# Optimization experiments

Measured on AMD Instinct MI355X. Metric: run time of the kernel, lower is better.

## Reference

```python
import jax, jax.numpy as jnp
import numpy as np

C_S, C_Z, H, P_QK, P_V, L = 384, 128, 12, 4, 8, 768
D = C_S // H
OUT_DIM = C_S + H * P_V * 3 + H * C_Z


def setup_inputs() -> dict:
    key = jax.random.key(0)
    ks = jax.random.split(key, 16)
    sc = lambda fan_in: 1.0 / np.sqrt(fan_in)
    inp = {
        'single': jax.random.normal(ks[0], (L, C_S), jnp.float32),
        'pair': jax.random.normal(ks[1], (L, L, C_Z), jnp.float32),
        'rots': jax.random.normal(ks[2], (L, 3, 3), jnp.float32),
        'trans': jax.random.normal(ks[3], (L, 3), jnp.float32),
        'ln_g': jnp.ones((C_S,), jnp.float32),
        'ln_b': jnp.zeros((C_S,), jnp.float32),
        'Wq': jax.random.normal(ks[4], (C_S, C_S), jnp.float32) * sc(C_S),
        'Wk': jax.random.normal(ks[5], (C_S, C_S), jnp.float32) * sc(C_S),
        'Wv': jax.random.normal(ks[6], (C_S, C_S), jnp.float32) * sc(C_S),
        'Wqp': jax.random.normal(ks[7], (C_S, H * P_QK * 3), jnp.float32) * sc(C_S),
        'bqp': jnp.zeros((H * P_QK * 3,), jnp.float32),
        'Wkp': jax.random.normal(ks[8], (C_S, H * P_QK * 3), jnp.float32) * sc(C_S),
        'bkp': jnp.zeros((H * P_QK * 3,), jnp.float32),
        'Wvp': jax.random.normal(ks[9], (C_S, H * P_V * 3), jnp.float32) * sc(C_S),
        'bvp': jnp.zeros((H * P_V * 3,), jnp.float32),
        'Wpb': jax.random.normal(ks[10], (C_Z, H), jnp.float32) * sc(C_Z),
        'head_weights': jnp.zeros((H,), jnp.float32),
        'Wo': jax.random.normal(ks[11], (OUT_DIM, C_S), jnp.float32) * sc(OUT_DIM),
        'bo': jnp.zeros((C_S,), jnp.float32),
    }
    return inp


def _layernorm(x, g, b, eps=1e-5):
    mu = x.mean(-1, keepdims=True)
    var = ((x - mu) ** 2).mean(-1, keepdims=True)
    return (x - mu) * jax.lax.rsqrt(var + eps) * g + b


def _apply_frames(pts, rots, trans):
    # pts: [L,H,P,3]; rotate each local point into global frame, then translate
    return jnp.einsum('lij,lhpj->lhpi', rots, pts) + trans[:, None, None, :]


def reference(single, pair, rots, trans, ln_g, ln_b, Wq, Wk, Wv, Wqp, bqp,
              Wkp, bkp, Wvp, bvp, Wpb, head_weights, Wo, bo):
    s = _layernorm(single, ln_g, ln_b)
    q = (s @ Wq).reshape(L, H, D)
    k = (s @ Wk).reshape(L, H, D)
    v = (s @ Wv).reshape(L, H, D)
    q_pts = (s @ Wqp + bqp).reshape(L, H, P_QK, 3)
    k_pts = (s @ Wkp + bkp).reshape(L, H, P_QK, 3)
    v_pts = (s @ Wvp + bvp).reshape(L, H, P_V, 3)

    q_g = _apply_frames(q_pts, rots, trans)
    k_g = _apply_frames(k_pts, rots, trans)
    v_g = _apply_frames(v_pts, rots, trans)

    # scalar attention logits [H, L, L]
    attn = jnp.einsum('ihd,jhd->hij', q, k) / np.sqrt(D).astype(np.float32)
    # point-distance bias: ||q_g_i - k_g_j||^2 summed over points -> [L,L,H]
    pt_diff = q_g[:, None] - k_g[None, :]            # [L,L,H,P,3]
    pt_dist_sq = (pt_diff ** 2).sum((-1, -2))        # [L,L,H]
    w_c = jax.nn.softplus(head_weights)
    attn = attn - 0.5 * w_c[:, None, None] * jnp.transpose(pt_dist_sq, (2, 0, 1))
    attn = attn + jnp.einsum('ijc,ch->hij', pair, Wpb)
    attn = jax.nn.softmax(attn, axis=-1)

    out_scalar = jnp.einsum('hij,jhd->ihd', attn, v).reshape(L, C_S)
    out_pts_g = jnp.einsum('hij,jhpc->ihpc', attn, v_g)  # [L,H,Pv,3]
    flat_pts = out_pts_g.reshape(L, H * P_V, 3) - trans[:, None, :]
    # inverse rotation = transpose: einsum with swapped rot indices
    out_pts_l = jnp.einsum('lji,lnj->lni', rots, flat_pts).reshape(L, H * P_V * 3)
    out_pair = jnp.einsum('hij,ijc->ihc', attn, pair).reshape(L, H * C_Z)

    cat = jnp.concatenate([out_scalar, out_pts_l, out_pair], axis=-1)
    return cat @ Wo + bo
```

## Files before the change

kernel.cpp:

```cpp
#include <hip/hip_runtime.h>
#include <math.h>

#define LSEQ 768
#define CS   384
#define CZ   128
#define NH   12
#define OUTD 2208
#define PROJW 1728
#define LL2  (LSEQ*LSEQ)

__device__ __forceinline__ float waveSum(float v){
#pragma unroll
  for (int o = 32; o > 0; o >>= 1) v += __shfl_down(v, o, 64);
  return v;
}

__global__ __launch_bounds__(128) void k_layernorm(
    const float* __restrict__ x, const float* __restrict__ g,
    const float* __restrict__ b, float* __restrict__ s){
  int i = blockIdx.x, t = threadIdx.x;
  const float* row = x + (size_t)i*CS;
  float v0 = row[t], v1 = row[t+128], v2 = row[t+256];
  float sum = v0+v1+v2;
  float sq  = v0*v0+v1*v1+v2*v2;
  float ws1 = waveSum(sum), ws2 = waveSum(sq);
  __shared__ float red[4];
  int w = t>>6, lane = t&63;
  if (lane == 0){ red[w] = ws1; red[w+2] = ws2; }
  __syncthreads();
  float mu   = (red[0]+red[1]) * (1.f/CS);
  float var  = (red[2]+red[3]) * (1.f/CS) - mu*mu;
  float rstd = rsqrtf(var + 1e-5f);
  float* o = s + (size_t)i*CS;
  o[t]     = (v0-mu)*rstd*g[t]     + b[t];
  o[t+128] = (v1-mu)*rstd*g[t+128] + b[t+128];
  o[t+256] = (v2-mu)*rstd*g[t+256] + b[t+256];
}

__global__ void k_wcat(const float* __restrict__ Wq, const float* __restrict__ Wk,
                       const float* __restrict__ Wv, const float* __restrict__ Wqp,
                       const float* __restrict__ Wkp, const float* __restrict__ Wvp,
                       const float* __restrict__ bqp, const float* __restrict__ bkp,
                       const float* __restrict__ bvp,
                       float* __restrict__ wcat, float* __restrict__ bcat){
  int idx = blockIdx.x*256 + threadIdx.x;
  if (idx < PROJW){
    float bv = 0.f;
    if (idx >= 1440)      bv = bvp[idx-1440];
    else if (idx >= 1296) bv = bkp[idx-1296];
    else if (idx >= 1152) bv = bqp[idx-1152];
    bcat[idx] = bv;
  }
  if (idx >= 384*PROJW) return;
  int r = idx / PROJW, c = idx % PROJW;
  float v;
  if (c < 384)       v = Wq[r*384 + c];
  else if (c < 768)  v = Wk[r*384 + c-384];
  else if (c < 1152) v = Wv[r*384 + c-768];
  else if (c < 1296) v = Wqp[r*144 + c-1152];
  else if (c < 1440) v = Wkp[r*144 + c-1296];
  else               v = Wvp[r*288 + c-1440];
  wcat[idx] = v;
}

__global__ __launch_bounds__(256) void k_gemm(
    const float* __restrict__ A, const float* __restrict__ B,
    const float* __restrict__ bias, float* __restrict__ C,
    int M, int N, int K, int kChunk){
  __shared__ float As[16][65];
  __shared__ float Bs[16][65];
  int j0 = blockIdx.x*64, i0 = blockIdx.y*64;
  int kBeg = blockIdx.z * kChunk;
  int t = threadIdx.x, tx = t & 15, ty = t >> 4;
  int arow = t >> 2, ak = (t & 3) * 4;
  int brow = t >> 4, bcol = (t & 15) * 4;
  float acc[4][4] = {};
  for (int kb = kBeg; kb < kBeg + kChunk; kb += 16){
    float4 av = *(const float4*)(A + (size_t)(i0+arow)*K + kb + ak);
    As[ak+0][arow]=av.x; As[ak+1][arow]=av.y; As[ak+2][arow]=av.z; As[ak+3][arow]=av.w;
    float4 bv = make_float4(0.f,0.f,0.f,0.f);
    if (j0 + bcol < N) bv = *(const float4*)(B + (size_t)(kb+brow)*N + j0 + bcol);
    Bs[brow][bcol+0]=bv.x; Bs[brow][bcol+1]=bv.y; Bs[brow][bcol+2]=bv.z; Bs[brow][bcol+3]=bv.w;
    __syncthreads();
#pragma unroll
    for (int kk = 0; kk < 16; ++kk){
      float a0=As[kk][ty*4+0],a1=As[kk][ty*4+1],a2=As[kk][ty*4+2],a3=As[kk][ty*4+3];
      float b0=Bs[kk][tx*4+0],b1=Bs[kk][tx*4+1],b2=Bs[kk][tx*4+2],b3=Bs[kk][tx*4+3];
      acc[0][0]+=a0*b0; acc[0][1]+=a0*b1; acc[0][2]+=a0*b2; acc[0][3]+=a0*b3;
      acc[1][0]+=a1*b0; acc[1][1]+=a1*b1; acc[1][2]+=a1*b2; acc[1][3]+=a1*b3;
      acc[2][0]+=a2*b0; acc[2][1]+=a2*b1; acc[2][2]+=a2*b2; acc[2][3]+=a2*b3;
      acc[3][0]+=a3*b0; acc[3][1]+=a3*b1; acc[3][2]+=a3*b2; acc[3][3]+=a3*b3;
    }
    __syncthreads();
  }
  bool noSplit = (gridDim.z == 1);
#pragma unroll
  for (int r = 0; r < 4; ++r){
    int i = i0 + ty*4 + r;
#pragma unroll
    for (int c = 0; c < 4; ++c){
      int j = j0 + tx*4 + c;
      if (j < N){
        float v = acc[r][c];
        if (noSplit && bias) v += bias[j];
        C[(size_t)i*N + j] = v;
      }
    }
  }
}

__global__ __launch_bounds__(256) void k_gemmWo(
    const float* __restrict__ A, const float* __restrict__ B, float* __restrict__ C){
  __shared__ float As[8][132];
  __shared__ float Bs[8][132];
  const int j0 = blockIdx.x*128, i0 = blockIdx.y*128;
  const int kBeg = blockIdx.z*184;
  const int t = threadIdx.x;
  const int arow = t >> 1, akq = (t & 1)*4;
  const int bk = t >> 5, bn = (t & 31)*4;
  const int tx = t & 15, ty = t >> 4;
  float acc[8][8] = {};
  for (int kb = kBeg; kb < kBeg+184; kb += 8){
    float4 av = *(const float4*)(A + (size_t)(i0+arow)*OUTD + kb + akq);
    float4 bv = *(const float4*)(B + (size_t)(kb+bk)*CS + j0 + bn);
    As[akq+0][arow]=av.x; As[akq+1][arow]=av.y; As[akq+2][arow]=av.z; As[akq+3][arow]=av.w;
    *(float4*)(&Bs[bk][bn]) = bv;
    __syncthreads();
#pragma unroll
    for (int k = 0; k < 8; ++k){
      float a[8], b[8];
      *(float4*)(a)   = *(const float4*)(&As[k][ty*8]);
      *(float4*)(a+4) = *(const float4*)(&As[k][ty*8+4]);
      *(float4*)(b)   = *(const float4*)(&Bs[k][tx*8]);
      *(float4*)(b+4) = *(const float4*)(&Bs[k][tx*8+4]);
#pragma unroll
      for (int r = 0; r < 8; ++r)
#pragma unroll
        for (int c = 0; c < 8; ++c) acc[r][c] += a[r]*b[c];
    }
    __syncthreads();
  }
  float* out = C + (size_t)blockIdx.z*LSEQ*CS;
#pragma unroll
  for (int r = 0; r < 8; ++r){
    float* o = out + (size_t)(i0+ty*8+r)*CS + j0 + tx*8;
    *(float4*)(o)   = make_float4(acc[r][0],acc[r][1],acc[r][2],acc[r][3]);
    *(float4*)(o+4) = make_float4(acc[r][4],acc[r][5],acc[r][6],acc[r][7]);
  }
}

__global__ __launch_bounds__(256) void k_prep(
    float* __restrict__ proj, const float* __restrict__ rots,
    const float* __restrict__ trans, const float* __restrict__ hw,
    float* __restrict__ Qa, float* __restrict__ Ka, float* __restrict__ nrm){
  int i = blockIdx.x, t = threadIdx.x;
  __shared__ float wcl[12];
  __shared__ float qg[144], kg[144];
  if (t < 12) wcl[t] = log1pf(__expf(hw[t]));
  float* prow = proj + (size_t)i*PROJW;
  if (t < 192){
    const float* R  = rots + i*9;
    const float* tr = trans + i*3;
    int off = (t < 48) ? (1152 + t*3) : ((t < 96) ? (1296 + (t-48)*3) : (1440 + (t-96)*3));
    float x = prow[off], y = prow[off+1], z = prow[off+2];
    float gx = R[0]*x + R[1]*y + R[2]*z + tr[0];
    float gy = R[3]*x + R[4]*y + R[5]*z + tr[1];
    float gz = R[6]*x + R[7]*y + R[8]*z + tr[2];
    if (t < 48){ qg[t*3]=gx; qg[t*3+1]=gy; qg[t*3+2]=gz; }
    else if (t < 96){ int u=t-48; kg[u*3]=gx; kg[u*3+1]=gy; kg[u*3+2]=gz; }
    else { prow[off]=gx; prow[off+1]=gy; prow[off+2]=gz; }
  }
  __syncthreads();
  const float isq = 0.17677669529663687f;
  for (int idx = t; idx < 576; idx += 256){
    int h = idx/48, d = idx%48;
    float qv = 0.f, kv = 0.f;
    if (d < 32){ qv = prow[h*32 + d]*isq; kv = prow[384 + h*32 + d]; }
    else if (d < 44){ qv = qg[h*12 + (d-32)]*wcl[h]; kv = kg[h*12 + (d-32)]; }
    Qa[((size_t)h*LSEQ + i)*48 + d] = qv;
    Ka[((size_t)h*LSEQ + i)*48 + d] = kv;
  }
  if (t < 24){
    int h = t % 12; int isK = (t >= 12) ? 1 : 0;
    const float* g = isK ? kg : qg;
    float sum = 0.f;
#pragma unroll
    for (int d = 0; d < 12; ++d){ float v = g[h*12+d]; sum += v*v; }
    nrm[((size_t)(isK*12 + h))*LSEQ + i] = -0.5f*wcl[h]*sum;
  }
}

__global__ __launch_bounds__(256) void k_qkaug(
    const float* __restrict__ Qa, const float* __restrict__ Ka,
    const float* __restrict__ nrm, float* __restrict__ logits){
  int j0 = blockIdx.x*64, i0 = blockIdx.y*64, h = blockIdx.z;
  __shared__ float Qs[64*49], Ks[64*49];
  __shared__ float nq[64], nk[64];
  int t = threadIdx.x;
  for (int idx = t; idx < 768; idx += 256){
    int row = idx/12, c4 = (idx%12)*4;
    float4 qv = *(const float4*)(Qa + ((size_t)h*LSEQ + i0+row)*48 + c4);
    Qs[row*49+c4]=qv.x; Qs[row*49+c4+1]=qv.y; Qs[row*49+c4+2]=qv.z; Qs[row*49+c4+3]=qv.w;
    float4 kv = *(const float4*)(Ka + ((size_t)h*LSEQ + j0+row)*48 + c4);
    Ks[row*49+c4]=kv.x; Ks[row*49+c4+1]=kv.y; Ks[row*49+c4+2]=kv.z; Ks[row*49+c4+3]=kv.w;
  }
  if (t < 64) nq[t] = nrm[(size_t)h*LSEQ + i0 + t];
  else if (t < 128) nk[t-64] = nrm[(size_t)(12+h)*LSEQ + j0 + (t-64)];
  __syncthreads();
  int tx = t & 15, ty = t >> 4;
  float acc[4][4] = {};
#pragma unroll 4
  for (int k = 0; k < 44; ++k){
    float a0=Qs[(ty*4+0)*49+k], a1=Qs[(ty*4+1)*49+k], a2=Qs[(ty*4+2)*49+k], a3=Qs[(ty*4+3)*49+k];
    float b0=Ks[(tx*4+0)*49+k], b1=Ks[(tx*4+1)*49+k], b2=Ks[(tx*4+2)*49+k], b3=Ks[(tx*4+3)*49+k];
    acc[0][0]+=a0*b0; acc[0][1]+=a0*b1; acc[0][2]+=a0*b2; acc[0][3]+=a0*b3;
    acc[1][0]+=a1*b0; acc[1][1]+=a1*b1; acc[1][2]+=a1*b2; acc[1][3]+=a1*b3;
    acc[2][0]+=a2*b0; acc[2][1]+=a2*b1; acc[2][2]+=a2*b2; acc[2][3]+=a2*b3;
    acc[3][0]+=a3*b0; acc[3][1]+=a3*b1; acc[3][2]+=a3*b2; acc[3][3]+=a3*b3;
  }
  float nqa[4] = {nq[ty*4], nq[ty*4+1], nq[ty*4+2], nq[ty*4+3]};
  float nk0=nk[tx*4], nk1=nk[tx*4+1], nk2=nk[tx*4+2], nk3=nk[tx*4+3];
#pragma unroll
  for (int r = 0; r < 4; ++r){
    float4 o = make_float4(acc[r][0]+nqa[r]+nk0, acc[r][1]+nqa[r]+nk1,
                           acc[r][2]+nqa[r]+nk2, acc[r][3]+nqa[r]+nk3);
    *(float4*)(logits + ((size_t)h*LSEQ + i0+ty*4+r)*LSEQ + j0 + tx*4) = o;
  }
}

__global__ __launch_bounds__(256) void k_pairfused(
    const float* __restrict__ pair, const float* __restrict__ Wpb,
    float* __restrict__ attn,
    float* __restrict__ cat){
  const int i = blockIdx.x, t = threadIdx.x;
  __shared__ __align__(16) float Sb[12*776];
  const float4* prowf4 = (const float4*)(pair + (size_t)i*LSEQ*CZ);

  for (int rr = 0; rr < 3; ++rr){
    const int r = t + rr*256;
    const float4* src = prowf4 + (size_t)r*32;
    float acc[12] = {0.f,0.f,0.f,0.f,0.f,0.f,0.f,0.f,0.f,0.f,0.f,0.f};
#pragma unroll 2
    for (int c4 = 0; c4 < 32; ++c4){
      float4 pv = src[c4];
      const float* wq = Wpb + c4*48;
#pragma unroll
      for (int h = 0; h < 12; ++h)
        acc[h] += pv.x*wq[h] + pv.y*wq[h+12] + pv.z*wq[h+24] + pv.w*wq[h+36];
    }
#pragma unroll
    for (int h = 0; h < 12; ++h) Sb[h*776 + r] = acc[h];
  }
  __syncthreads();

  const int w = t >> 6, lane = t & 63;
#pragma unroll
  for (int e = 0; e < 3; ++e){
    const int h = w*3 + e;
    float* lg = attn + (size_t)h*LL2 + (size_t)i*LSEQ;
    float4 xa = *(const float4*)(lg + lane*4);
    float4 xb = *(const float4*)(lg + 256 + lane*4);
    float4 xc = *(const float4*)(lg + 512 + lane*4);
    float4 ba = *(const float4*)(Sb + h*776 + lane*4);
    float4 bb = *(const float4*)(Sb + h*776 + 256 + lane*4);
    float4 bc = *(const float4*)(Sb + h*776 + 512 + lane*4);
    xa.x+=ba.x; xa.y+=ba.y; xa.z+=ba.z; xa.w+=ba.w;
    xb.x+=bb.x; xb.y+=bb.y; xb.z+=bb.z; xb.w+=bb.w;
    xc.x+=bc.x; xc.y+=bc.y; xc.z+=bc.z; xc.w+=bc.w;
    float m = fmaxf(fmaxf(fmaxf(xa.x,xa.y),fmaxf(xa.z,xa.w)),
             fmaxf(fmaxf(fmaxf(xb.x,xb.y),fmaxf(xb.z,xb.w)),
                   fmaxf(fmaxf(xc.x,xc.y),fmaxf(xc.z,xc.w))));
#pragma unroll
    for (int ms = 32; ms > 0; ms >>= 1) m = fmaxf(m, __shfl_xor(m, ms));
    xa.x=__expf(xa.x-m); xa.y=__expf(xa.y-m); xa.z=__expf(xa.z-m); xa.w=__expf(xa.w-m);
    xb.x=__expf(xb.x-m); xb.y=__expf(xb.y-m); xb.z=__expf(xb.z-m); xb.w=__expf(xb.w-m);
    xc.x=__expf(xc.x-m); xc.y=__expf(xc.y-m); xc.z=__expf(xc.z-m); xc.w=__expf(xc.w-m);
    float s = xa.x+xa.y+xa.z+xa.w + xb.x+xb.y+xb.z+xb.w + xc.x+xc.y+xc.z+xc.w;
#pragma unroll
    for (int ms = 32; ms > 0; ms >>= 1) s += __shfl_xor(s, ms);
    float inv = 1.f/s;
    xa.x*=inv; xa.y*=inv; xa.z*=inv; xa.w*=inv;
    xb.x*=inv; xb.y*=inv; xb.z*=inv; xb.w*=inv;
    xc.x*=inv; xc.y*=inv; xc.z*=inv; xc.w*=inv;
    *(float4*)(Sb + h*776 + lane*4)       = xa;
    *(float4*)(Sb + h*776 + 256 + lane*4) = xb;
    *(float4*)(Sb + h*776 + 512 + lane*4) = xc;
    *(float4*)(lg + lane*4)       = xa;
    *(float4*)(lg + 256 + lane*4) = xb;
    *(float4*)(lg + 512 + lane*4) = xc;
  }
  __syncthreads();

  const int cq = t & 31, rp = t >> 5;
  float4 acc3[12];
#pragma unroll
  for (int h = 0; h < 12; ++h) acc3[h] = make_float4(0.f,0.f,0.f,0.f);
  for (int g = 0; g < 24; ++g){
    const int r0 = g*32 + rp*4;
    float4 pv0 = prowf4[(size_t)(r0+0)*32 + cq];
    float4 pv1 = prowf4[(size_t)(r0+1)*32 + cq];
    float4 pv2 = prowf4[(size_t)(r0+2)*32 + cq];
    float4 pv3 = prowf4[(size_t)(r0+3)*32 + cq];
#pragma unroll
    for (int h = 0; h < 12; ++h){
      float4 p4 = *(const float4*)(Sb + h*776 + r0);
      acc3[h].x += pv0.x*p4.x + pv1.x*p4.y + pv2.x*p4.z + pv3.x*p4.w;
      acc3[h].y += pv0.y*p4.x + pv1.y*p4.y + pv2.y*p4.z + pv3.y*p4.w;
      acc3[h].z += pv0.z*p4.x + pv1.z*p4.y + pv2.z*p4.z + pv3.z*p4.w;
      acc3[h].w += pv0.w*p4.x + pv1.w*p4.y + pv2.w*p4.z + pv3.w*p4.w;
    }
  }
#pragma unroll
  for (int h = 0; h < 12; ++h){
    acc3[h].x += __shfl_xor(acc3[h].x, 32);
    acc3[h].y += __shfl_xor(acc3[h].y, 32);
    acc3[h].z += __shfl_xor(acc3[h].z, 32);
    acc3[h].w += __shfl_xor(acc3[h].w, 32);
  }
  __syncthreads();
  if (lane < 32){
#pragma unroll
    for (int h = 0; h < 12; ++h)
      *(float4*)(Sb + w*1536 + h*128 + cq*4) = acc3[h];
  }
  __syncthreads();
  float* crow = cat + (size_t)i*OUTD + 672;
  for (int o = t; o < 1536; o += 256)
    crow[o] = Sb[o] + Sb[1536+o] + Sb[3072+o] + Sb[4608+o];
}

__global__ __launch_bounds__(256) void k_pv(
    const float* __restrict__ attn, const float* __restrict__ proj,
    const float* __restrict__ rots, const float* __restrict__ trans,
    float* __restrict__ cat){
  int h = blockIdx.y, i0 = blockIdx.x*32;
  __shared__ float As[32][34];
  __shared__ float Bs[32][57];
  __shared__ float pts[32][24];
  int t = threadIdx.x, tx = t & 15, ty = t >> 4;
  float acc[2][4] = {};
  for (int kb = 0; kb < LSEQ; kb += 32){
    __syncthreads();
    {
      int row = t >> 3, k4 = (t & 7)*4;
      float4 av = *(const float4*)(attn + ((size_t)h*LSEQ + i0 + row)*LSEQ + kb + k4);
      As[k4+0][row]=av.x; As[k4+1][row]=av.y; As[k4+2][row]=av.z; As[k4+3][row]=av.w;
    }
    for (int idx = t; idx < 32*56; idx += 256){
      int kk = idx/56, n = idx%56;
      const float* prow = proj + (size_t)(kb+kk)*PROJW;
      Bs[kk][n] = (n < 32) ? prow[768 + h*32 + n] : prow[1440 + h*24 + (n-32)];
    }
    __syncthreads();
    if (tx < 14){
#pragma unroll
      for (int kk = 0; kk < 32; ++kk){
        float a0 = As[kk][ty*2], a1 = As[kk][ty*2+1];
        float b[4]; *(float4*)b = *(const float4*)(&Bs[kk][tx*4]);
#pragma unroll
        for (int c = 0; c < 4; ++c){ acc[0][c] += a0*b[c]; acc[1][c] += a1*b[c]; }
      }
    }
  }
  __syncthreads();
  if (tx < 14){
#pragma unroll
    for (int r = 0; r < 2; ++r){
      int i = i0 + ty*2 + r;
#pragma unroll
      for (int c = 0; c < 4; ++c){
        int n = tx*4 + c;
        if (n < 32) cat[(size_t)i*OUTD + h*32 + n] = acc[r][c];
        else pts[ty*2+r][n-32] = acc[r][c];
      }
    }
  }
  __syncthreads();
  {
    int row = t >> 3, p = t & 7;
    int i = i0 + row;
    const float* R = rots + i*9; const float* tr = trans + i*3;
    float x = pts[row][p*3]   - tr[0];
    float y = pts[row][p*3+1] - tr[1];
    float z = pts[row][p*3+2] - tr[2];
    float* o = cat + (size_t)i*OUTD + 384 + h*24 + p*3;
    o[0] = R[0]*x + R[3]*y + R[6]*z;
    o[1] = R[1]*x + R[4]*y + R[7]*z;
    o[2] = R[2]*x + R[5]*y + R[8]*z;
  }
}

__global__ __launch_bounds__(256) void k_reduce(
    const float* __restrict__ part, const float* __restrict__ bias,
    float* __restrict__ out){
  int idx = blockIdx.x*256 + threadIdx.x;
  if (idx >= LSEQ*CS) return;
  float v = bias[idx % CS];
#pragma unroll
  for (int z = 0; z < 12; ++z) v += part[(size_t)z*LSEQ*CS + idx];
  out[idx] = v;
}

extern "C" void kernel_launch(void* const* d_in, const int* in_sizes, int n_in,
                              void* d_out, int out_size, void* d_ws, size_t ws_size,
                              hipStream_t stream){
  const float* single = (const float*)d_in[0];
  const float* pair   = (const float*)d_in[1];
  const float* rots   = (const float*)d_in[2];
  const float* trans  = (const float*)d_in[3];
  const float* ln_g   = (const float*)d_in[4];
  const float* ln_b   = (const float*)d_in[5];
  const float* Wq  = (const float*)d_in[6];
  const float* Wk  = (const float*)d_in[7];
  const float* Wv  = (const float*)d_in[8];
  const float* Wqp = (const float*)d_in[9];
  const float* bqp = (const float*)d_in[10];
  const float* Wkp = (const float*)d_in[11];
  const float* bkp = (const float*)d_in[12];
  const float* Wvp = (const float*)d_in[13];
  const float* bvp = (const float*)d_in[14];
  const float* Wpb = (const float*)d_in[15];
  const float* hw  = (const float*)d_in[16];
  const float* Wo  = (const float*)d_in[17];
  const float* bo  = (const float*)d_in[18];
  float* out = (float*)d_out;

  float* ws = (float*)d_ws;
  float* s    = ws;
  float* wcat = ws + 294912;
  float* bcat = ws + 958464;
  float* Qa   = ws;
  float* Ka   = ws + 442368;
  float* nrm  = ws + 884736;
  float* proj = ws + 960256;
  float* attn = ws + 2287360;
  float* cat  = ws + 9365248;
  float* part = attn;

  k_layernorm<<<LSEQ, 128, 0, stream>>>(single, ln_g, ln_b, s);
  k_wcat<<<(384*PROJW+255)/256, 256, 0, stream>>>(Wq,Wk,Wv,Wqp,Wkp,Wvp,bqp,bkp,bvp,wcat,bcat);
  k_gemm<<<dim3(27,12,1), 256, 0, stream>>>(s, wcat, bcat, proj, 768, PROJW, 384, 384);
  k_prep<<<LSEQ, 256, 0, stream>>>(proj, rots, trans, hw, Qa, Ka, nrm);
  k_qkaug<<<dim3(12,12,12), 256, 0, stream>>>(Qa, Ka, nrm, attn);
  k_pairfused<<<LSEQ, 256, 0, stream>>>(pair, Wpb, attn, cat);
  k_pv<<<dim3(24, NH), 256, 0, stream>>>(attn, proj, rots, trans, cat);
  k_gemmWo<<<dim3(3,6,12), 256, 0, stream>>>(cat, Wo, part);
  k_reduce<<<(LSEQ*CS+255)/256, 256, 0, stream>>>(part, bo, out);
}
```

Baseline: 379.6 us.

## Merge layernorm and weight concat launches, prefetch logits, shrink PV tiles

Merges the layernorm and weight-concatenation kernels into one launch, with block index selecting the role, to save a kernel launch. In the pair-fused kernel the logits rows are loaded before the pair-bias projection so their latency overlaps that work, and two loops get more unrolling. The PV kernel halves its row tile to 16, doubling grid size for better occupancy across CUs, at the cost of reloading the B tile twice as often. These add register pressure and some redundant proj reads.

```diff
diff --git a/kernel.cpp b/kernel.cpp
--- a/kernel.cpp
+++ b/kernel.cpp
@@ -15,35 +15,37 @@
   return v;
 }
 
-__global__ __launch_bounds__(128) void k_layernorm(
+__global__ __launch_bounds__(128) void k_lnwcat(
     const float* __restrict__ x, const float* __restrict__ g,
-    const float* __restrict__ b, float* __restrict__ s){
-  int i = blockIdx.x, t = threadIdx.x;
-  const float* row = x + (size_t)i*CS;
-  float v0 = row[t], v1 = row[t+128], v2 = row[t+256];
-  float sum = v0+v1+v2;
-  float sq  = v0*v0+v1*v1+v2*v2;
-  float ws1 = waveSum(sum), ws2 = waveSum(sq);
-  __shared__ float red[4];
-  int w = t>>6, lane = t&63;
-  if (lane == 0){ red[w] = ws1; red[w+2] = ws2; }
-  __syncthreads();
-  float mu   = (red[0]+red[1]) * (1.f/CS);
-  float var  = (red[2]+red[3]) * (1.f/CS) - mu*mu;
-  float rstd = rsqrtf(var + 1e-5f);
-  float* o = s + (size_t)i*CS;
-  o[t]     = (v0-mu)*rstd*g[t]     + b[t];
-  o[t+128] = (v1-mu)*rstd*g[t+128] + b[t+128];
-  o[t+256] = (v2-mu)*rstd*g[t+256] + b[t+256];
-}
-
-__global__ void k_wcat(const float* __restrict__ Wq, const float* __restrict__ Wk,
-                       const float* __restrict__ Wv, const float* __restrict__ Wqp,
-                       const float* __restrict__ Wkp, const float* __restrict__ Wvp,
-                       const float* __restrict__ bqp, const float* __restrict__ bkp,
-                       const float* __restrict__ bvp,
-                       float* __restrict__ wcat, float* __restrict__ bcat){
-  int idx = blockIdx.x*256 + threadIdx.x;
+    const float* __restrict__ b, float* __restrict__ s,
+    const float* __restrict__ Wq, const float* __restrict__ Wk,
+    const float* __restrict__ Wv, const float* __restrict__ Wqp,
+    const float* __restrict__ Wkp, const float* __restrict__ Wvp,
+    const float* __restrict__ bqp, const float* __restrict__ bkp,
+    const float* __restrict__ bvp,
+    float* __restrict__ wcat, float* __restrict__ bcat){
+  int blk = blockIdx.x, t = threadIdx.x;
+  if (blk < LSEQ){
+    int i = blk;
+    const float* row = x + (size_t)i*CS;
+    float v0 = row[t], v1 = row[t+128], v2 = row[t+256];
+    float sum = v0+v1+v2;
+    float sq  = v0*v0+v1*v1+v2*v2;
+    float ws1 = waveSum(sum), ws2 = waveSum(sq);
+    __shared__ float red[4];
+    int w = t>>6, lane = t&63;
+    if (lane == 0){ red[w] = ws1; red[w+2] = ws2; }
+    __syncthreads();
+    float mu   = (red[0]+red[1]) * (1.f/CS);
+    float var  = (red[2]+red[3]) * (1.f/CS) - mu*mu;
+    float rstd = rsqrtf(var + 1e-5f);
+    float* o = s + (size_t)i*CS;
+    o[t]     = (v0-mu)*rstd*g[t]     + b[t];
+    o[t+128] = (v1-mu)*rstd*g[t+128] + b[t+128];
+    o[t+256] = (v2-mu)*rstd*g[t+256] + b[t+256];
+    return;
+  }
+  int idx = (blk - LSEQ)*128 + t;
   if (idx < PROJW){
     float bv = 0.f;
     if (idx >= 1440)      bv = bvp[idx-1440];
@@ -235,12 +237,26 @@
   const int i = blockIdx.x, t = threadIdx.x;
   __shared__ __align__(16) float Sb[12*776];
   const float4* prowf4 = (const float4*)(pair + (size_t)i*LSEQ*CZ);
+  const int w = t >> 6, lane = t & 63;
+
+  float* lg0 = attn + (size_t)(w*3+0)*LL2 + (size_t)i*LSEQ;
+  float* lg1 = attn + (size_t)(w*3+1)*LL2 + (size_t)i*LSEQ;
+  float* lg2 = attn + (size_t)(w*3+2)*LL2 + (size_t)i*LSEQ;
+  float4 X00 = *(const float4*)(lg0 + lane*4);
+  float4 X01 = *(const float4*)(lg0 + 256 + lane*4);
+  float4 X02 = *(const float4*)(lg0 + 512 + lane*4);
+  float4 X10 = *(const float4*)(lg1 + lane*4);
+  float4 X11 = *(const float4*)(lg1 + 256 + lane*4);
+  float4 X12 = *(const float4*)(lg1 + 512 + lane*4);
+  float4 X20 = *(const float4*)(lg2 + lane*4);
+  float4 X21 = *(const float4*)(lg2 + 256 + lane*4);
+  float4 X22 = *(const float4*)(lg2 + 512 + lane*4);
 
   for (int rr = 0; rr < 3; ++rr){
     const int r = t + rr*256;
     const float4* src = prowf4 + (size_t)r*32;
     float acc[12] = {0.f,0.f,0.f,0.f,0.f,0.f,0.f,0.f,0.f,0.f,0.f,0.f};
-#pragma unroll 2
+#pragma unroll 8
     for (int c4 = 0; c4 < 32; ++c4){
       float4 pv = src[c4];
       const float* wq = Wpb + c4*48;
@@ -253,14 +269,13 @@
   }
   __syncthreads();
 
-  const int w = t >> 6, lane = t & 63;
 #pragma unroll
   for (int e = 0; e < 3; ++e){
     const int h = w*3 + e;
-    float* lg = attn + (size_t)h*LL2 + (size_t)i*LSEQ;
-    float4 xa = *(const float4*)(lg + lane*4);
-    float4 xb = *(const float4*)(lg + 256 + lane*4);
-    float4 xc = *(const float4*)(lg + 512 + lane*4);
+    float* lg = (e == 0) ? lg0 : ((e == 1) ? lg1 : lg2);
+    float4 xa = (e == 0) ? X00 : ((e == 1) ? X10 : X20);
+    float4 xb = (e == 0) ? X01 : ((e == 1) ? X11 : X21);
+    float4 xc = (e == 0) ? X02 : ((e == 1) ? X12 : X22);
     float4 ba = *(const float4*)(Sb + h*776 + lane*4);
     float4 bb = *(const float4*)(Sb + h*776 + 256 + lane*4);
     float4 bc = *(const float4*)(Sb + h*776 + 512 + lane*4);
@@ -295,6 +310,7 @@
   float4 acc3[12];
 #pragma unroll
   for (int h = 0; h < 12; ++h) acc3[h] = make_float4(0.f,0.f,0.f,0.f);
+#pragma unroll 2
   for (int g = 0; g < 24; ++g){
     const int r0 = g*32 + rp*4;
     float4 pv0 = prowf4[(size_t)(r0+0)*32 + cq];
@@ -333,18 +349,18 @@
     const float* __restrict__ attn, const float* __restrict__ proj,
     const float* __restrict__ rots, const float* __restrict__ trans,
     float* __restrict__ cat){
-  int h = blockIdx.y, i0 = blockIdx.x*32;
-  __shared__ float As[32][34];
+  int h = blockIdx.y, i0 = blockIdx.x*16;
+  __shared__ float As[32][17];
   __shared__ float Bs[32][57];
-  __shared__ float pts[32][24];
+  __shared__ float pts[16][24];
   int t = threadIdx.x, tx = t & 15, ty = t >> 4;
-  float acc[2][4] = {};
+  float acc[4] = {};
   for (int kb = 0; kb < LSEQ; kb += 32){
     __syncthreads();
     {
-      int row = t >> 3, k4 = (t & 7)*4;
-      float4 av = *(const float4*)(attn + ((size_t)h*LSEQ + i0 + row)*LSEQ + kb + k4);
-      As[k4+0][row]=av.x; As[k4+1][row]=av.y; As[k4+2][row]=av.z; As[k4+3][row]=av.w;
+      int row = t >> 4, k2 = (t & 15)*2;
+      float2 av = *(const float2*)(attn + ((size_t)h*LSEQ + i0 + row)*LSEQ + kb + k2);
+      As[k2][row] = av.x; As[k2+1][row] = av.y;
     }
     for (int idx = t; idx < 32*56; idx += 256){
       int kk = idx/56, n = idx%56;
@@ -355,28 +371,24 @@
     if (tx < 14){
 #pragma unroll
       for (int kk = 0; kk < 32; ++kk){
-        float a0 = As[kk][ty*2], a1 = As[kk][ty*2+1];
+        float a = As[kk][ty];
         float b[4]; *(float4*)b = *(const float4*)(&Bs[kk][tx*4]);
-#pragma unroll
-        for (int c = 0; c < 4; ++c){ acc[0][c] += a0*b[c]; acc[1][c] += a1*b[c]; }
+        acc[0] += a*b[0]; acc[1] += a*b[1]; acc[2] += a*b[2]; acc[3] += a*b[3];
       }
     }
   }
   __syncthreads();
   if (tx < 14){
-#pragma unroll
-    for (int r = 0; r < 2; ++r){
-      int i = i0 + ty*2 + r;
-#pragma unroll
-      for (int c = 0; c < 4; ++c){
-        int n = tx*4 + c;
-        if (n < 32) cat[(size_t)i*OUTD + h*32 + n] = acc[r][c];
-        else pts[ty*2+r][n-32] = acc[r][c];
-      }
-    }
-  }
-  __syncthreads();
-  {
+    int i = i0 + ty;
+#pragma unroll
+    for (int c = 0; c < 4; ++c){
+      int n = tx*4 + c;
+      if (n < 32) cat[(size_t)i*OUTD + h*32 + n] = acc[c];
+      else pts[ty][n-32] = acc[c];
+    }
+  }
+  __syncthreads();
+  if (t < 128){
     int row = t >> 3, p = t & 7;
     int i = i0 + row;
     const float* R = rots + i*9; const float* tr = trans + i*3;
@@ -437,13 +449,14 @@
   float* cat  = ws + 9365248;
   float* part = attn;
 
-  k_layernorm<<<LSEQ, 128, 0, stream>>>(single, ln_g, ln_b, s);
-  k_wcat<<<(384*PROJW+255)/256, 256, 0, stream>>>(Wq,Wk,Wv,Wqp,Wkp,Wvp,bqp,bkp,bvp,wcat,bcat);
+  int wcatBlocks = (384*PROJW + 127)/128;
+  k_lnwcat<<<LSEQ + wcatBlocks, 128, 0, stream>>>(single, ln_g, ln_b, s,
+      Wq, Wk, Wv, Wqp, Wkp, Wvp, bqp, bkp, bvp, wcat, bcat);
   k_gemm<<<dim3(27,12,1), 256, 0, stream>>>(s, wcat, bcat, proj, 768, PROJW, 384, 384);
   k_prep<<<LSEQ, 256, 0, stream>>>(proj, rots, trans, hw, Qa, Ka, nrm);
   k_qkaug<<<dim3(12,12,12), 256, 0, stream>>>(Qa, Ka, nrm, attn);
   k_pairfused<<<LSEQ, 256, 0, stream>>>(pair, Wpb, attn, cat);
-  k_pv<<<dim3(24, NH), 256, 0, stream>>>(attn, proj, rots, trans, cat);
+  k_pv<<<dim3(48, NH), 256, 0, stream>>>(attn, proj, rots, trans, cat);
   k_gemmWo<<<dim3(3,6,12), 256, 0, stream>>>(cat, Wo, part);
   k_reduce<<<(LSEQ*CS+255)/256, 256, 0, stream>>>(part, bo, out);
 }
```

Measured after the change: 371.0 us. 1.02x faster.
